# Optimization experiments

Measured on AMD Instinct MI355X. Metric: run time of the kernel, lower is better.

Reference implementation:

```python
import jax, jax.numpy as jnp
import numpy as np

E = 8            # num experts
CAP_FACTOR = 1.5
K_THRESH = 0.8
BAL_ALPHA = 0.005
REG_ALPHA = 1e-6
BN_EPS = 1e-5
POOL = 16


def setup_inputs() -> dict:
    key = jax.random.key(0)
    ks = jax.random.split(key, 8)
    B, H, L, D = 128, 1024, 512, 1024
    return {
        "x": jax.random.normal(ks[0], (B, H, L), jnp.float32),
        "conv_w": jax.random.normal(ks[1], (64, H, 3), jnp.float32) / np.float32(np.sqrt(3 * H)),
        "conv_b": jnp.zeros((64,), jnp.float32),
        "bn_gamma": jnp.ones((64 * POOL,), jnp.float32),
        "bn_beta": jnp.zeros((64 * POOL,), jnp.float32),
        "fc1_w": jax.random.normal(ks[2], (128, 64 * POOL), jnp.float32) / np.float32(np.sqrt(64 * POOL)),
        "fc1_b": jnp.zeros((128,), jnp.float32),
        "fc2_w": jax.random.normal(ks[3], (E, 128), jnp.float32) / np.float32(np.sqrt(128)),
        "fc2_b": jnp.zeros((E,), jnp.float32),
        "exp_w": jax.random.normal(ks[4], (E, H, D), jnp.float32) / np.float32(np.sqrt(H)),
        "exp_b": jnp.zeros((E, D), jnp.float32),
    }


def _forward(x, conv_w, conv_b, bn_gamma, bn_beta, fc1_w, fc1_b, fc2_w, fc2_b, exp_w, exp_b):
    B, H, L = x.shape
    # ---- router: Conv1d(H->64,k=3,p=1) -> GELU -> AdaptiveAvgPool1d(16) -> Flatten -> BN -> FC -> GELU -> FC -> softmax
    h = jax.lax.conv_general_dilated(x, conv_w, (1,), ((1, 1),),
                                     dimension_numbers=("NCH", "OIH", "NCH"))
    h = jax.nn.gelu(h + conv_b[None, :, None], approximate=False)          # [B,64,L]; torch GELU is exact erf
    h = h.reshape(B, 64, POOL, L // POOL).mean(-1).reshape(B, 64 * POOL)   # adaptive avg pool (L%16==0) + flatten
    mu, var = h.mean(0), h.var(0)                                          # training-mode (Sync)BatchNorm: batch stats
    h = (h - mu) / jnp.sqrt(var + BN_EPS) * bn_gamma + bn_beta
    h = jax.nn.gelu(h @ fc1_w.T + fc1_b, approximate=False)
    rw = jax.nn.softmax(h @ fc2_w.T + fc2_b, axis=1)                       # [B,E]; expert dropout = identity (eval)
    # ---- dynamic k: smallest k s.t. cumsum of sorted probs > threshold; only max over batch is used
    topk_w, topk_idx = jax.lax.top_k(rw, E)                                # full descending sort
    cum = jnp.cumsum(topk_w, axis=1)
    over = cum > K_THRESH
    k_per = jnp.where(jnp.any(over, axis=1), jnp.argmax(over, axis=1) + 1, E)
    max_k = jnp.max(jnp.clip(k_per, 1, E))
    col_valid = jnp.arange(E)[None, :] < max_k                             # broadcast [B,E]; cols >= max_k unused
    assign = jnp.where(col_valid, topk_idx, -1)
    # ---- capacity enforcement: per expert keep the `capacity` highest-weight assignments, drop the rest (-1)
    capacity = max(1, int(B * CAP_FACTOR / E))
    flat_idx, flat_w = assign.reshape(-1), topk_w.reshape(-1)              # row-major [B*E], matches torch flatten

    def keep_for_expert(e):
        m = flat_idx == e
        order = jnp.argsort(-jnp.where(m, flat_w, -jnp.inf))               # descending within expert e
        ranks = jnp.zeros_like(order).at[order].set(jnp.arange(order.shape[0]))
        return m & (ranks < capacity)

    keep = jax.vmap(keep_for_expert)(jnp.arange(E))                        # [E, B*E]
    counts = keep.sum(axis=1).astype(jnp.float32)                          # == bincount of valid final indices
    final_idx = jnp.where(jnp.any(keep, axis=0), flat_idx, -1).reshape(B, E)
    # ---- experts: mean-pool over length, per-expert Linear(H->D); gather each sample's selected experts
    pooled = x.mean(axis=2)                                                # [B,H]
    y = jnp.einsum("bh,ehd->bed", pooled, exp_w) + exp_b[None]             # [B,E,D] all-expert outputs
    outputs = jnp.take_along_axis(y, jnp.clip(final_idx, 0)[..., None], axis=1)
    outputs = jnp.where(final_idx[..., None] >= 0, outputs, 0.0)           # dropped slots contribute zeros
    # ---- combine: softmax over the max_k slots; dropped (-1) slots enter softmax with logit 0, as in torch
    logits = jnp.where(col_valid, topk_w * (final_idx >= 0), -jnp.inf)
    norm_w = jax.nn.softmax(logits, axis=1)                                # [B,E]
    pooler = jnp.einsum("bkd,bk->bd", outputs, norm_w)                     # [B,D]
    # ---- losses / stats
    usage = rw.mean(0)
    reg = jnp.sum(exp_w * exp_w) + jnp.sum(exp_b * exp_b)                  # sum ||param||_2^2 over expert params
    added_loss = BAL_ALPHA * jnp.var(usage, ddof=1) + REG_ALPHA * reg      # torch.var is unbiased
    return pooler, added_loss, usage, counts


def reference(x, conv_w, conv_b, bn_gamma, bn_beta, fc1_w, fc1_b, fc2_w, fc2_b, exp_w, exp_b):
    return _forward(x, conv_w, conv_b, bn_gamma, bn_beta, fc1_w, fc1_b, fc2_w, fc2_b, exp_w, exp_b)
```

## Files before the change

### kernel.cpp

```cpp
#include <hip/hip_runtime.h>
#include <hip/hip_bf16.h>
#include <math.h>

#define NB 128
#define NH 1024
#define NL 512
#define OC 64
#define NE 8
#define ND 1024
#define CAPACITY 24

static const size_t WS_PART  = 0;
static const size_t WS_WSEP  = 1048576;
static const size_t WS_PXT   = 2097152;
static const size_t WS_HPOOL = 2228224;
static const size_t WS_SCALE = 2359296;
static const size_t WS_SHIFT = 2360320;
static const size_t WS_TKW   = 2377728;
static const size_t WS_TKI   = 2378752;
static const size_t WS_USAGE = 2379784;
static const size_t WS_VARU  = 2379792;
static const size_t WS_REG   = 2379793;
static const size_t WS_CNT   = 2379794;
static const size_t WS_WMAT  = 2380832;
static const size_t WS_RW    = 2381856;
static const size_t WS_KP    = 2382880;

typedef __attribute__((ext_vector_type(8))) short bf16x8;
typedef __attribute__((ext_vector_type(4))) float f32x4;

__device__ __forceinline__ float gelu_exact(float v) {
    return 0.5f * v * (1.0f + erff(v * 0.70710678118654752440f));
}

__device__ __forceinline__ unsigned short f2bf_rne(float f) {
    unsigned int u = __float_as_uint(f);
    unsigned int r = u + 0x7FFFu + ((u >> 16) & 1u);
    return (unsigned short)(r >> 16);
}
__device__ __forceinline__ float bf2f(unsigned short h) {
    return __uint_as_float(((unsigned int)h) << 16);
}

__device__ __forceinline__ unsigned cvtpk_bf16(float a, float b) {
    unsigned r;
    asm("v_cvt_pk_bf16_f32 %0, %1, %2" : "=v"(r) : "v"(a), "v"(b));
    return r;
}

__device__ __forceinline__ void gload_lds16(const void* gsrc, void* ldst) {
    __builtin_amdgcn_global_load_lds(
        (const __attribute__((address_space(1))) void*)gsrc,
        (__attribute__((address_space(3))) void*)ldst,
        16, 0, 0);
}

__global__ __launch_bounds__(256) void k_wsplit(const float* __restrict__ cw, float* __restrict__ ws)
{
    if (blockIdx.x == 0 && threadIdx.x == 0) ws[WS_REG] = 0.0f;
    unsigned short* wsep = (unsigned short*)(ws + WS_WSEP);
    int i = blockIdx.x * 256 + threadIdx.x;
    int lane = i & 63;
    int split = (i >> 6) & 1;
    int mt = (i >> 7) & 3;
    int rest = i >> 9;
    int j = rest % 3;
    int it = rest / 3;
    int o = mt * 16 + (lane & 15);
    int hb = it * 32 + ((lane >> 4) << 3);
    unsigned short v8[8];
#pragma unroll
    for (int e = 0; e < 8; ++e) {
        float v = cw[((size_t)o * 1024 + hb + e) * 3 + j];
        unsigned short hi = f2bf_rne(v);
        v8[e] = split ? f2bf_rne(v - bf2f(hi)) : hi;
    }
    *(uint4*)(wsep + ((size_t)((it * 3 + j) * 4 + mt) * 2 + split) * 512 + lane * 8) = *(uint4*)v8;
}

__device__ __forceinline__ void cvt_unit(unsigned int* X, int lq, int h4,
                                         const float4* v, float* sh)
{
    sh[0] = sh[1] = sh[2] = sh[3] = 0.f;
#pragma unroll
    for (int i = 0; i < 4; ++i) {
        float a0 = ((const float*)&v[0])[i];
        float a1 = ((const float*)&v[1])[i];
        float a2 = ((const float*)&v[2])[i];
        float a3 = ((const float*)&v[3])[i];
        sh[0] += a0; sh[1] += a1; sh[2] += a2; sh[3] += a3;
        unsigned h01 = cvtpk_bf16(a0, a1);
        unsigned h23 = cvtpk_bf16(a2, a3);
        float r0 = a0 - __uint_as_float(h01 << 16);
        float r1 = a1 - __uint_as_float(h01 & 0xFFFF0000u);
        float r2 = a2 - __uint_as_float(h23 << 16);
        float r3 = a3 - __uint_as_float(h23 & 0xFFFF0000u);
        unsigned l01 = cvtpk_bf16(r0, r1);
        unsigned l23 = cvtpk_bf16(r2, r3);
        int r = lq * 4 + i;
        unsigned int* dst = X + r * 34 + ((2 * h4) ^ ((r & 3) << 2));
        *(uint2*)dst = make_uint2(h01, h23);
        *(uint2*)(dst + 16) = make_uint2(l01, l23);
    }
}

__global__ __launch_bounds__(256, 2) void k_convmfma(const float* __restrict__ x,
                                                     const float* __restrict__ cb,
                                                     float* __restrict__ ws)
{
    __shared__ unsigned short Ab[2][12288];
    __shared__ unsigned int X[136 * 34];
    __shared__ float xs2[3][128];
    __shared__ float scb[64];

    const int lc = blockIdx.x, b = blockIdx.y;
    const int l0 = lc * 128;
    const int tid = threadIdx.x;
    const int wv = tid >> 6, lane = tid & 63;
    const int h4 = tid & 7;
    const int lqi = 1 + (tid >> 3);
    const bool has_halo = (tid < 16);
    const int lqh = (tid < 8) ? 0 : 33;
    const bool halo_ok = (tid < 8) ? (lc > 0) : (lc < 3);

    const unsigned short* wsg = (const unsigned short*)(ws + WS_WSEP);
    const float* xbase = x + (size_t)b * (NH * NL);
    float* poolp = ws + WS_PART + ((size_t)(lc * 128 + b)) * 1024;

    if (tid < 64) scb[tid] = cb[tid];

    f32x4 acc[4][2];
#pragma unroll
    for (int mt = 0; mt < 4; ++mt)
#pragma unroll
        for (int nt = 0; nt < 2; ++nt) acc[mt][nt] = (f32x4){0.f, 0.f, 0.f, 0.f};

    float4 xA[4], hA[4], xB[4], hB[4];

    auto xload = [&](int itL, float4* xc, float4* hc) {
        const int hn = itL * 32;
        const float* p = xbase + (size_t)(hn + h4 * 4) * NL + (l0 - 4 + lqi * 4);
#pragma unroll
        for (int jj = 0; jj < 4; ++jj) xc[jj] = *(const float4*)(p + jj * NL);
        if (has_halo) {
            int gl = l0 - 4 + lqh * 4;
#pragma unroll
            for (int jj = 0; jj < 4; ++jj)
                hc[jj] = halo_ok ? *(const float4*)(xbase + (size_t)(hn + h4 * 4 + jj) * NL + gl)
                                 : make_float4(0.f, 0.f, 0.f, 0.f);
        }
    };

    auto adma = [&](int itL) {
        const unsigned short* src = wsg + (size_t)itL * 12288;
        unsigned short* dst = Ab[itL & 1];
#pragma unroll
        for (int c = 0; c < 6; ++c)
            gload_lds16(src + (size_t)(c * 256 + tid) * 8, dst + (size_t)(c * 256 + tid) * 8);
    };

    auto body = [&](int it, float4* xc, float4* hc) {
        {
            float sh[4];
            cvt_unit(X, lqi, h4, xc, sh);
#pragma unroll
            for (int jj = 0; jj < 4; ++jj) {
                float s = sh[jj];
                s += __shfl_xor(s, 8, 64);
                s += __shfl_xor(s, 16, 64);
                s += __shfl_xor(s, 32, 64);
                if ((lane >> 3) == 0) xs2[it % 3][wv * 32 + h4 * 4 + jj] = s;
            }
            if (has_halo) { float d[4]; cvt_unit(X, lqh, h4, hc, d); }
        }
        __syncthreads();
        if (it > 0 && tid < 32) {
            const float* S = xs2[(it - 1) % 3];
            poolp[(it - 1) * 32 + tid] = S[tid] + S[32 + tid] + S[64 + tid] + S[96 + tid];
        }
        if (it < 30) xload(it + 2, xc, hc);
        if (it < 31) adma(it + 1);
        const int g4 = (lane >> 4) << 2;
        const unsigned short* An = Ab[it & 1] + lane * 8;
#pragma unroll
        for (int j = 0; j < 3; ++j) {
            bf16x8 Bh[2], Bl[2];
#pragma unroll
            for (int nt = 0; nt < 2; ++nt) {
                int rx = 3 + j + wv * 32 + nt * 16 + (lane & 15);
                const unsigned int* bp = X + rx * 34 + (g4 ^ ((rx & 3) << 2));
                Bh[nt] = *(const bf16x8*)bp;
                Bl[nt] = *(const bf16x8*)(bp + 16);
            }
#pragma unroll
            for (int mt = 0; mt < 4; ++mt) {
                bf16x8 Ah = *(const bf16x8*)(An + (size_t)((j * 4 + mt) * 2) * 512);
                bf16x8 Al = *(const bf16x8*)(An + (size_t)((j * 4 + mt) * 2 + 1) * 512);
#pragma unroll
                for (int nt = 0; nt < 2; ++nt) {
                    acc[mt][nt] = __builtin_amdgcn_mfma_f32_16x16x32_bf16(Ah, Bh[nt], acc[mt][nt], 0, 0, 0);
                    acc[mt][nt] = __builtin_amdgcn_mfma_f32_16x16x32_bf16(Ah, Bl[nt], acc[mt][nt], 0, 0, 0);
                    acc[mt][nt] = __builtin_amdgcn_mfma_f32_16x16x32_bf16(Al, Bh[nt], acc[mt][nt], 0, 0, 0);
                }
            }
        }
        __syncthreads();
    };

    adma(0);
    xload(0, xA, hA);
    xload(1, xB, hB);

    for (int it2 = 0; it2 < 32; it2 += 2) {
        body(it2, xA, hA);
        body(it2 + 1, xB, hB);
    }
    if (tid < 32) {
        const float* S = xs2[31 % 3];
        poolp[31 * 32 + tid] = S[tid] + S[32 + tid] + S[64 + tid] + S[96 + tid];
    }

    {
        const int g = lane >> 4, cidx = lane & 15;
#pragma unroll
        for (int mt = 0; mt < 4; ++mt) {
            float s[4];
#pragma unroll
            for (int r = 0; r < 4; ++r) {
                int o = mt * 16 + g * 4 + r;
                float bo = scb[o];
                s[r] = gelu_exact(acc[mt][0][r] + bo) + gelu_exact(acc[mt][1][r] + bo);
            }
#pragma unroll
            for (int m = 1; m < 16; m <<= 1) {
#pragma unroll
                for (int r = 0; r < 4; ++r) s[r] += __shfl_xor(s[r], m, 64);
            }
            if (cidx == 0) {
#pragma unroll
                for (int r = 0; r < 4; ++r) {
                    int o = mt * 16 + g * 4 + r;
                    ws[WS_HPOOL + (size_t)b * 1024 + o * 16 + lc * 4 + wv] = s[r] * (1.0f / 32.0f);
                }
            }
        }
    }
}

__global__ __launch_bounds__(256) void k_mid(const float* __restrict__ g,
                                             const float* __restrict__ bet,
                                             float* __restrict__ ws)
{
    int bx = blockIdx.x;
    if (bx < 512) {
        int id = bx * 256 + threadIdx.x;
        int b = id >> 10, h = id & 1023;
        float s = 0.0f;
#pragma unroll
        for (int lcc = 0; lcc < 4; lcc++) s += ws[WS_PART + ((size_t)(lcc * 128 + b)) * 1024 + h];
        ws[WS_PXT + (size_t)h * 128 + b] = s * (1.0f / 512.0f);
    } else {
        int f = (bx - 512) * 256 + threadIdx.x;
        const float* hp = ws + WS_HPOOL;
        float s = 0.0f;
        for (int b = 0; b < 128; b++) s += hp[(size_t)b * 1024 + f];
        float mu = s * (1.0f / 128.0f);
        float v = 0.0f;
        for (int b = 0; b < 128; b++) { float d = hp[(size_t)b * 1024 + f] - mu; v += d * d; }
        float var = v * (1.0f / 128.0f);
        float sc = g[f] / sqrtf(var + 1e-5f);
        ws[WS_SCALE + f] = sc;
        ws[WS_SHIFT + f] = bet[f] - mu * sc;
    }
}

__global__ __launch_bounds__(256) void k_fused(const float* __restrict__ w1,
                                               const float* __restrict__ b1,
                                               const float* __restrict__ w2,
                                               const float* __restrict__ b2,
                                               const float* __restrict__ ew,
                                               const float* __restrict__ eb,
                                               float* __restrict__ ws)
{
    __shared__ float smem[5376];
    const int bx = blockIdx.x;
    const int tid = threadIdx.x;

    if (bx < 512) {
        float* a_s = smem;
        float* b_s = smem + 4096;
        float* red2 = smem + 5120;
        const int e = bx >> 6, dt = (bx >> 1) & 31, ks = bx & 1;
        const int tb = tid >> 3, td = tid & 7;
        float acc[4][4];
#pragma unroll
        for (int i = 0; i < 4; i++)
#pragma unroll
            for (int j = 0; j < 4; j++) acc[i][j] = 0.0f;
        float ssq = 0.0f;

        const float* pxt = ws + WS_PXT;
        for (int kt = 0; kt < 512; kt += 32) {
            __syncthreads();
            for (int idx = tid; idx < 4096; idx += 256) {
                int kk = idx >> 7, bb = idx & 127;
                a_s[kk * 128 + bb] = pxt[(size_t)(ks * 512 + kt + kk) * 128 + bb];
            }
            for (int idx = tid; idx < 1024; idx += 256) {
                int kk = idx >> 5, d = idx & 31;
                float v = ew[(size_t)e * 1048576 + (size_t)(ks * 512 + kt + kk) * 1024 + dt * 32 + d];
                b_s[kk * 32 + d] = v;
                ssq += v * v;
            }
            __syncthreads();
#pragma unroll 4
            for (int kk = 0; kk < 32; kk++) {
                float4 av = *(const float4*)&a_s[kk * 128 + tb * 4];
                float4 bv = *(const float4*)&b_s[kk * 32 + td * 4];
                float aa[4] = {av.x, av.y, av.z, av.w};
                float bb4[4] = {bv.x, bv.y, bv.z, bv.w};
#pragma unroll
                for (int i = 0; i < 4; i++)
#pragma unroll
                    for (int j = 0; j < 4; j++) acc[i][j] = fmaf(aa[i], bb4[j], acc[i][j]);
            }
        }
        float* outp = ws + WS_PART + ((size_t)(ks * 8 + e) * 128) * 1024 + dt * 32;
#pragma unroll
        for (int i = 0; i < 4; i++) {
            int bb = tb * 4 + i;
            *(float4*)(outp + (size_t)bb * 1024 + td * 4) =
                make_float4(acc[i][0], acc[i][1], acc[i][2], acc[i][3]);
        }
        if (bx == 0)
            for (int i = tid; i < 8192; i += 256) { float v = eb[i]; ssq += v * v; }
        red2[tid] = ssq;
        __syncthreads();
        for (int off = 128; off > 0; off >>= 1) {
            if (tid < off) red2[tid] += red2[tid + off];
            __syncthreads();
        }
        if (tid == 0) atomicAdd(ws + WS_REG, red2[0]);
    } else {
        float* hb  = smem;
        float* red = smem + 1024;
        float* ha  = smem + 1280;
        float* w2s = smem + 1408;
        float* lg  = smem + 2432;
        const int b = bx - 512;
        const float* hp = ws + WS_HPOOL + (size_t)b * 1024;
        for (int k = tid; k < 1024; k += 256)
            hb[k] = hp[k] * ws[WS_SCALE + k] + ws[WS_SHIFT + k];
        for (int i = tid; i < 1024; i += 256) w2s[i] = w2[i];
        __syncthreads();
        int o = tid & 127, kh = tid >> 7;
        const float4* wrp = (const float4*)(w1 + (size_t)o * 1024 + kh * 512);
        const float* hx = hb + kh * 512;
        float acc = 0.0f;
#pragma unroll 4
        for (int k = 0; k < 128; k++) {
            float4 w = wrp[k];
            acc = fmaf(hx[4 * k], w.x, acc);     acc = fmaf(hx[4 * k + 1], w.y, acc);
            acc = fmaf(hx[4 * k + 2], w.z, acc); acc = fmaf(hx[4 * k + 3], w.w, acc);
        }
        red[tid] = acc;
        __syncthreads();
        if (tid < 128)
            ha[tid] = gelu_exact(red[tid] + red[tid + 128] + b1[tid]);
        __syncthreads();
        if (tid < 8) {
            float a2 = b2[tid];
            for (int k = 0; k < 128; k++) a2 = fmaf(ha[k], w2s[tid * 128 + k], a2);
            lg[tid] = a2;
        }
        __syncthreads();
        if (tid == 0) {
            float rw[8];
            float m = -1e30f;
#pragma unroll
            for (int e = 0; e < 8; e++) m = fmaxf(m, lg[e]);
            float s = 0.0f;
#pragma unroll
            for (int e = 0; e < 8; e++) { rw[e] = expf(lg[e] - m); s += rw[e]; }
            float inv = 1.0f / s;
#pragma unroll
            for (int e = 0; e < 8; e++) { rw[e] *= inv; ws[WS_RW + b * 8 + e] = rw[e]; }
            float tw[8]; int ti[8]; unsigned used = 0;
#pragma unroll
            for (int r = 0; r < 8; r++) {
                float bv = -1e30f; int bi = 0;
#pragma unroll
                for (int e = 0; e < 8; e++) {
                    bool take = !((used >> e) & 1u) && (rw[e] > bv);
                    bv = take ? rw[e] : bv;
                    bi = take ? e : bi;
                }
                used |= (1u << bi);
                tw[r] = bv; ti[r] = bi;
            }
            float cum = 0.0f; int kp = 8;
#pragma unroll
            for (int r = 0; r < 8; r++) {
                cum += tw[r];
                if (cum > 0.8f) { kp = r + 1; break; }
            }
#pragma unroll
            for (int r = 0; r < 8; r++) {
                ws[WS_TKW + b * 8 + r] = tw[r];
                ((int*)ws)[WS_TKI + b * 8 + r] = ti[r];
            }
            ((int*)ws)[WS_KP + b] = kp;
        }
    }
}

__global__ __launch_bounds__(128) void k_route(float* __restrict__ ws)
{
    __shared__ float tkw_s[1024];
    __shared__ int   tki_s[1024];
    __shared__ int   keep_s[1024];
    __shared__ float wv_s[128];
    __shared__ int   sv_s[128];
    __shared__ float usg[8];
    __shared__ int   cnt_s[8];
    __shared__ int   mk;

    const int tid = threadIdx.x;
    const int b = tid;
    if (tid == 0) mk = 0;
    if (tid < 8) cnt_s[tid] = 0;
    __syncthreads();
    atomicMax(&mk, ((const int*)ws)[WS_KP + b]);
#pragma unroll
    for (int r = 0; r < 8; r++) {
        tkw_s[b * 8 + r] = ws[WS_TKW + b * 8 + r];
        tki_s[b * 8 + r] = ((const int*)ws)[WS_TKI + b * 8 + r];
    }
    __syncthreads();
    const int maxk = mk;

    if (tid < 8) {
        float s2 = 0.0f;
        for (int bb = 0; bb < 128; bb++) s2 += ws[WS_RW + bb * 8 + tid];
        float u = s2 * (1.0f / 128.0f);
        usg[tid] = u;
        ws[WS_USAGE + tid] = u;
    }
    __syncthreads();
    if (tid == 0) {
        float mu = 0.0f;
#pragma unroll
        for (int e = 0; e < 8; e++) mu += usg[e];
        mu *= (1.0f / 8.0f);
        float v = 0.0f;
#pragma unroll
        for (int e = 0; e < 8; e++) { float d = usg[e] - mu; v += d * d; }
        ws[WS_VARU] = v * (1.0f / 7.0f);
    }

    for (int e = 0; e < 8; ++e) {
        float myw = 0.0f; int mys = -1;
        for (int k = 0; k < maxk; k++)
            if (tki_s[b * 8 + k] == e) { myw = tkw_s[b * 8 + k]; mys = b * 8 + k; }
        wv_s[b] = myw; sv_s[b] = mys;
        __syncthreads();
        if (mys >= 0) {
            int rank = 0;
            for (int b2 = 0; b2 < 128; b2++) {
                int s2 = sv_s[b2];
                if (s2 >= 0) {
                    float w2v = wv_s[b2];
                    if (w2v > myw || (w2v == myw && s2 < mys)) rank++;
                }
            }
            int kept = (rank < CAPACITY) ? 1 : 0;
            keep_s[mys] = kept;
            if (kept) atomicAdd(&cnt_s[e], 1);
        }
        __syncthreads();
    }
    if (tid < 8) ws[WS_CNT + tid] = (float)cnt_s[tid];

    float lv[8]; int kept[8]; int idx[8];
#pragma unroll
    for (int k = 0; k < 8; k++) {
        if (k < maxk) {
            kept[k] = keep_s[b * 8 + k];
            idx[k] = tki_s[b * 8 + k];
            lv[k] = kept[k] ? tkw_s[b * 8 + k] : 0.0f;
        } else { kept[k] = 0; idx[k] = -1; lv[k] = -1e30f; }
    }
    float mx = -1e30f;
#pragma unroll
    for (int k = 0; k < 8; k++) if (k < maxk) mx = fmaxf(mx, lv[k]);
    float s3 = 0.0f; float ev[8];
#pragma unroll
    for (int k = 0; k < 8; k++) { ev[k] = (k < maxk) ? expf(lv[k] - mx) : 0.0f; s3 += ev[k]; }
    float inv3 = 1.0f / s3;
    float Wr[8] = {0, 0, 0, 0, 0, 0, 0, 0};
#pragma unroll
    for (int k = 0; k < 8; k++) {
        if (kept[k]) {
            float v = ev[k] * inv3;
#pragma unroll
            for (int e = 0; e < 8; e++) Wr[e] += (idx[k] == e) ? v : 0.0f;
        }
    }
#pragma unroll
    for (int e = 0; e < 8; e++) ws[WS_WMAT + b * 8 + e] = Wr[e];
}

__global__ __launch_bounds__(256) void k_final(const float* __restrict__ eb,
                                               const float* __restrict__ ws,
                                               float* __restrict__ out)
{
    int id = blockIdx.x * 256 + threadIdx.x;
    int b = id >> 8, dq = id & 255;
    const float* wm = ws + WS_WMAT + b * 8;
    const float* Y = ws + WS_PART;
    float4 s = make_float4(0.f, 0.f, 0.f, 0.f);
#pragma unroll
    for (int e = 0; e < 8; e++) {
        float4 y0 = *(const float4*)(Y + ((size_t)e * 128 + b) * 1024 + dq * 4);
        float4 y1 = *(const float4*)(Y + ((size_t)(8 + e) * 128 + b) * 1024 + dq * 4);
        float4 bb = *(const float4*)(eb + (size_t)e * 1024 + dq * 4);
        float w = wm[e];
        s.x += w * (y0.x + y1.x + bb.x);
        s.y += w * (y0.y + y1.y + bb.y);
        s.z += w * (y0.z + y1.z + bb.z);
        s.w += w * (y0.w + y1.w + bb.w);
    }
    *(float4*)(out + (size_t)b * 1024 + dq * 4) = s;
    if (blockIdx.x == 0) {
        int t = threadIdx.x;
        if (t == 0) out[131072] = 0.005f * ws[WS_VARU] + 1e-6f * ws[WS_REG];
        else if (t >= 1 && t < 9)  out[131072 + t] = ws[WS_USAGE + t - 1];
        else if (t >= 9 && t < 17) out[131072 + t] = ws[WS_CNT + t - 9];
    }
}

extern "C" void kernel_launch(void* const* d_in, const int* in_sizes, int n_in,
                              void* d_out, int out_size, void* d_ws, size_t ws_size,
                              hipStream_t stream)
{
    const float* x   = (const float*)d_in[0];
    const float* cw  = (const float*)d_in[1];
    const float* cb  = (const float*)d_in[2];
    const float* bng = (const float*)d_in[3];
    const float* bnb = (const float*)d_in[4];
    const float* f1w = (const float*)d_in[5];
    const float* f1b = (const float*)d_in[6];
    const float* f2w = (const float*)d_in[7];
    const float* f2b = (const float*)d_in[8];
    const float* ew  = (const float*)d_in[9];
    const float* eb  = (const float*)d_in[10];
    float* ws  = (float*)d_ws;
    float* out = (float*)d_out;

    k_wsplit  <<<192, 256, 0, stream>>>(cw, ws);
    k_convmfma<<<dim3(4, 128), 256, 0, stream>>>(x, cb, ws);
    k_mid     <<<516, 256, 0, stream>>>(bng, bnb, ws);
    k_fused   <<<640, 256, 0, stream>>>(f1w, f1b, f2w, f2b, ew, eb, ws);
    k_route   <<<1, 128, 0, stream>>>(ws);
    k_final   <<<128, 256, 0, stream>>>(eb, ws, out);
}
```

Baseline: 319.0 us.

## Load conv weights directly into registers and double-buffer X tile to drop second barrier

Conv weight fragments were previously staged into LDS with async global-to-LDS copies. They are now read straight from global memory (L2-resident) into registers at the start of each iteration. The X tile in LDS is double-buffered, which lets the trailing __syncthreads per iteration be removed. This cuts LDS traffic and one barrier per step, at the cost of 24 extra bf16x8 VGPR fragments per thread and exposed global-load latency at the start of each iteration, which may pressure occupancy under launch_bounds(256,2).

```diff
diff --git a/kernel.cpp b/kernel.cpp
--- a/kernel.cpp
+++ b/kernel.cpp
@@ -46,13 +46,6 @@
     unsigned r;
     asm("v_cvt_pk_bf16_f32 %0, %1, %2" : "=v"(r) : "v"(a), "v"(b));
     return r;
-}
-
-__device__ __forceinline__ void gload_lds16(const void* gsrc, void* ldst) {
-    __builtin_amdgcn_global_load_lds(
-        (const __attribute__((address_space(1))) void*)gsrc,
-        (__attribute__((address_space(3))) void*)ldst,
-        16, 0, 0);
 }
 
 __global__ __launch_bounds__(256) void k_wsplit(const float* __restrict__ cw, float* __restrict__ ws)
@@ -108,8 +101,7 @@
                                                      const float* __restrict__ cb,
                                                      float* __restrict__ ws)
 {
-    __shared__ unsigned short Ab[2][12288];
-    __shared__ unsigned int X[136 * 34];
+    __shared__ unsigned int Xb[2][136 * 34];
     __shared__ float xs2[3][128];
     __shared__ float scb[64];
 
@@ -151,18 +143,22 @@
         }
     };
 
-    auto adma = [&](int itL) {
-        const unsigned short* src = wsg + (size_t)itL * 12288;
-        unsigned short* dst = Ab[itL & 1];
-#pragma unroll
-        for (int c = 0; c < 6; ++c)
-            gload_lds16(src + (size_t)(c * 256 + tid) * 8, dst + (size_t)(c * 256 + tid) * 8);
-    };
-
     auto body = [&](int it, float4* xc, float4* hc) {
+        unsigned int* Xw = Xb[it & 1];
+        bf16x8 Ar[3][4][2];
+        {
+            const unsigned short* abase = wsg + (size_t)it * 12288 + lane * 8;
+#pragma unroll
+            for (int j = 0; j < 3; ++j)
+#pragma unroll
+                for (int mt = 0; mt < 4; ++mt) {
+                    Ar[j][mt][0] = *(const bf16x8*)(abase + (size_t)((j * 8 + mt * 2) * 512));
+                    Ar[j][mt][1] = *(const bf16x8*)(abase + (size_t)((j * 8 + mt * 2 + 1) * 512));
+                }
+        }
         {
             float sh[4];
-            cvt_unit(X, lqi, h4, xc, sh);
+            cvt_unit(Xw, lqi, h4, xc, sh);
 #pragma unroll
             for (int jj = 0; jj < 4; ++jj) {
                 float s = sh[jj];
@@ -171,7 +167,7 @@
                 s += __shfl_xor(s, 32, 64);
                 if ((lane >> 3) == 0) xs2[it % 3][wv * 32 + h4 * 4 + jj] = s;
             }
-            if (has_halo) { float d[4]; cvt_unit(X, lqh, h4, hc, d); }
+            if (has_halo) { float d[4]; cvt_unit(Xw, lqh, h4, hc, d); }
         }
         __syncthreads();
         if (it > 0 && tid < 32) {
@@ -179,35 +175,28 @@
             poolp[(it - 1) * 32 + tid] = S[tid] + S[32 + tid] + S[64 + tid] + S[96 + tid];
         }
         if (it < 30) xload(it + 2, xc, hc);
-        if (it < 31) adma(it + 1);
         const int g4 = (lane >> 4) << 2;
-        const unsigned short* An = Ab[it & 1] + lane * 8;
 #pragma unroll
         for (int j = 0; j < 3; ++j) {
             bf16x8 Bh[2], Bl[2];
 #pragma unroll
             for (int nt = 0; nt < 2; ++nt) {
                 int rx = 3 + j + wv * 32 + nt * 16 + (lane & 15);
-                const unsigned int* bp = X + rx * 34 + (g4 ^ ((rx & 3) << 2));
+                const unsigned int* bp = Xw + rx * 34 + (g4 ^ ((rx & 3) << 2));
                 Bh[nt] = *(const bf16x8*)bp;
                 Bl[nt] = *(const bf16x8*)(bp + 16);
             }
 #pragma unroll
-            for (int mt = 0; mt < 4; ++mt) {
-                bf16x8 Ah = *(const bf16x8*)(An + (size_t)((j * 4 + mt) * 2) * 512);
-                bf16x8 Al = *(const bf16x8*)(An + (size_t)((j * 4 + mt) * 2 + 1) * 512);
+            for (int mt = 0; mt < 4; ++mt)
 #pragma unroll
                 for (int nt = 0; nt < 2; ++nt) {
-                    acc[mt][nt] = __builtin_amdgcn_mfma_f32_16x16x32_bf16(Ah, Bh[nt], acc[mt][nt], 0, 0, 0);
-                    acc[mt][nt] = __builtin_amdgcn_mfma_f32_16x16x32_bf16(Ah, Bl[nt], acc[mt][nt], 0, 0, 0);
-                    acc[mt][nt] = __builtin_amdgcn_mfma_f32_16x16x32_bf16(Al, Bh[nt], acc[mt][nt], 0, 0, 0);
+                    acc[mt][nt] = __builtin_amdgcn_mfma_f32_16x16x32_bf16(Ar[j][mt][0], Bh[nt], acc[mt][nt], 0, 0, 0);
+                    acc[mt][nt] = __builtin_amdgcn_mfma_f32_16x16x32_bf16(Ar[j][mt][0], Bl[nt], acc[mt][nt], 0, 0, 0);
+                    acc[mt][nt] = __builtin_amdgcn_mfma_f32_16x16x32_bf16(Ar[j][mt][1], Bh[nt], acc[mt][nt], 0, 0, 0);
                 }
-            }
-        }
-        __syncthreads();
+        }
     };
 
-    adma(0);
     xload(0, xA, hA);
     xload(1, xB, hB);
 
```

After: 312.0 us. -2.2%, faster.
